# Performance work log

Hardware: AMD Instinct MI355X
Metric: run time of the kernel (lower is better)

## Reference

```python
import jax, jax.numpy as jnp
import numpy as np
import math

_LINK_MASK_VALUE = -1000000000.0
B, N, HID, NH = 8, 1024, 1024, 4
HD = HID // NH


def setup_inputs() -> dict:
    key = jax.random.key(0)
    ks = jax.random.split(key, 8)
    features = jax.random.normal(ks[0], (B, N, HID), dtype=jnp.float32)
    valid_mask = jax.random.bernoulli(ks[1], 0.9, (B, N))
    s = 0.02
    Wq = jax.random.normal(ks[2], (HID, HID), dtype=jnp.float32) * s
    bq = jnp.zeros((HID,), dtype=jnp.float32)
    Wk = jax.random.normal(ks[3], (HID, HID), dtype=jnp.float32) * s
    bk = jnp.zeros((HID,), dtype=jnp.float32)
    Wg = jax.random.normal(ks[4], (HID, NH), dtype=jnp.float32) * s
    bg = jnp.zeros((NH,), dtype=jnp.float32)
    return {"features": features, "valid_mask": valid_mask,
            "Wq": Wq, "bq": bq, "Wk": Wk, "bk": bk, "Wg": Wg, "bg": bg}


def reference(features, valid_mask, Wq, bq, Wk, bk, Wg, bg):
    b, n, _ = features.shape
    Q = (features @ Wq + bq).reshape(b, n, NH, HD)
    K = (features @ Wk + bk).reshape(b, n, NH, HD)
    log_gates = jax.nn.log_softmax(features @ Wg + bg, axis=-1)  # (b, n, H)
    scores = jnp.einsum('bihd,bjhd->bijh', Q, K) / math.sqrt(HD)  # (b, i, j, H)
    triu = jnp.triu(jnp.ones((n, n), dtype=bool), k=1)            # (n, n)
    tvm = triu[None, :, :] & valid_mask[:, None, :]               # (b, i, j)
    row_dead = ~jnp.any(tvm, axis=2, keepdims=True)               # (b, i, 1)
    tvm = tvm | row_dead
    scores = jnp.where(tvm[..., None], scores, _LINK_MASK_VALUE)
    log_per_head = jax.nn.log_softmax(scores, axis=2)             # softmax over j
    log_per_head = jnp.where(row_dead[..., None], _LINK_MASK_VALUE, log_per_head)
    # mixture over heads with per-row gates
    log_links = jax.scipy.special.logsumexp(log_per_head + log_gates[:, :, None, :], axis=-1)
    return log_links
```

## Files before the change

kernel.cpp:

```cpp
#include <hip/hip_runtime.h>


typedef __attribute__((ext_vector_type(8))) short bf16x8;
typedef __attribute__((ext_vector_type(4))) short bf16x4;
typedef __attribute__((ext_vector_type(4))) float f32x4;
typedef __attribute__((ext_vector_type(16))) float f32x16;
typedef __attribute__((ext_vector_type(8))) int i32x8;

#define LB __launch_bounds__(256)

__device__ __forceinline__ short f2bf(float f) {
    unsigned u = __float_as_uint(f);
    u += 0x7fffu + ((u >> 16) & 1u);
    return (short)(u >> 16);
}

__device__ __forceinline__ void gld16(const void* g, void* l) {
    __builtin_amdgcn_global_load_lds(
        (const __attribute__((address_space(1))) unsigned int*)g,
        (__attribute__((address_space(3))) unsigned int*)l, 16, 0, 0);
}

__global__ LB void k_prep2(const float* __restrict__ feat, const float* __restrict__ Wg,
                           const float* __restrict__ bg, const float* __restrict__ Wq,
                           const float* __restrict__ Wk, char* __restrict__ X8,
                           float* __restrict__ lgA, char* __restrict__ W8) {
    __shared__ float tile[32][33];
    const int t = threadIdx.x;
    if (blockIdx.x < 2048) {
        int row = blockIdx.x * 4 + (t >> 6);
        int lane = t & 63;
        const float* f = feat + (size_t)row * 1024;
        float g0 = 0.f, g1 = 0.f, g2 = 0.f, g3 = 0.f;
#pragma unroll
        for (int tt = 0; tt < 4; ++tt) {
            int k = tt * 256 + lane * 4;
            float4 x = *(const float4*)&f[k];
            float4 w0 = *(const float4*)&Wg[(k + 0) * 4];
            float4 w1 = *(const float4*)&Wg[(k + 1) * 4];
            float4 w2 = *(const float4*)&Wg[(k + 2) * 4];
            float4 w3 = *(const float4*)&Wg[(k + 3) * 4];
            g0 += x.x * w0.x + x.y * w1.x + x.z * w2.x + x.w * w3.x;
            g1 += x.x * w0.y + x.y * w1.y + x.z * w2.y + x.w * w3.y;
            g2 += x.x * w0.z + x.y * w1.z + x.z * w2.z + x.w * w3.z;
            g3 += x.x * w0.w + x.y * w1.w + x.z * w2.w + x.w * w3.w;
            unsigned u01 = (unsigned)__builtin_amdgcn_cvt_pk_fp8_f32(x.x, x.y, 0, false);
            unsigned u23 = (unsigned)__builtin_amdgcn_cvt_pk_fp8_f32(x.z, x.w, 0, false);
            *(unsigned*)&X8[(size_t)row * 1024 + k] = (u01 & 0xffffu) | (u23 << 16);
        }
#pragma unroll
        for (int off = 32; off; off >>= 1) {
            g0 += __shfl_xor(g0, off); g1 += __shfl_xor(g1, off);
            g2 += __shfl_xor(g2, off); g3 += __shfl_xor(g3, off);
        }
        g0 += bg[0]; g1 += bg[1]; g2 += bg[2]; g3 += bg[3];
        float m = fmaxf(fmaxf(g0, g1), fmaxf(g2, g3));
        float s = __expf(g0 - m) + __expf(g1 - m) + __expf(g2 - m) + __expf(g3 - m);
        float ls = m + __logf(s);
        if (lane == 0) {
            float4 o = {g0 - ls, g1 - ls, g2 - ls, g3 - ls};
            *(float4*)&lgA[row * 4] = o;
        }
    } else {
        int bid = blockIdx.x - 2048;
        int n0 = (bid & 63) * 32, k0 = (bid >> 6) * 32;
        const float* W = (n0 < 1024) ? Wq : Wk;
        int nb = n0 & 1023;
        int tx = t & 31, ty = t >> 5;
#pragma unroll
        for (int jj = 0; jj < 4; ++jj) {
            int k = ty + jj * 8;
            tile[k][tx] = W[(size_t)(k0 + k) * 1024 + nb + tx];
        }
        __syncthreads();
#pragma unroll
        for (int jj = 0; jj < 4; ++jj) {
            int n = ty + jj * 8;
            float w16 = tile[tx][n] * 16.f;
            W8[(size_t)(n0 + n) * 1024 + k0 + tx] =
                (char)(__builtin_amdgcn_cvt_pk_fp8_f32(w16, w16, 0, false) & 0xff);
        }
    }
}

__device__ __forceinline__ i32x8 ldfrag8(const char* tb, int row, int khalf) {
    const int sw = (row >> 1) & 3;
    uint4 lo = *(const uint4*)&tb[row * 64 + (((khalf * 2 + 0) ^ sw) * 16)];
    uint4 hi = *(const uint4*)&tb[row * 64 + (((khalf * 2 + 1) ^ sw) * 16)];
    i32x8 r;
    r[0] = lo.x; r[1] = lo.y; r[2] = lo.z; r[3] = lo.w;
    r[4] = hi.x; r[5] = hi.y; r[6] = hi.z; r[7] = hi.w;
    return r;
}

__global__ __launch_bounds__(512, 2) void k_gemm(const char* __restrict__ X8,
                                                 const char* __restrict__ W8,
                                                 const float* __restrict__ bq,
                                                 const float* __restrict__ bk,
                                                 short* __restrict__ Qb,
                                                 short* __restrict__ Kb) {
    __shared__ char SM[3][32768];
    const int t = threadIdx.x;
    const int lane = t & 63, wid = t >> 6;
    const int wr = wid >> 2, wc = wid & 3;
    const int l31 = lane & 31, khalf = lane >> 5;
    const int wgid = (blockIdx.x & 7) * 32 + (blockIdx.x >> 3);
    const int m0t = (wgid >> 3) * 256, n0t = (wgid & 7) * 256;

    f32x16 acc[4][2] = {};

#define SGA(q, k1, dst)                                                         \
    { int s_ = (q) * 512 + t; int tr_ = s_ >> 2, c_ = s_ & 3;                   \
      gld16(&X8[(size_t)(m0t + tr_) * 1024 + (k1) + (((c_) ^ ((tr_ >> 1) & 3)) * 16)], \
            (dst) + s_ * 16); }
#define SGB(q, k1, dst)                                                         \
    { int s_ = (q) * 512 + t; int tr_ = s_ >> 2, c_ = s_ & 3;                   \
      gld16(&W8[(size_t)(n0t + tr_) * 1024 + (k1) + (((c_) ^ ((tr_ >> 1) & 3)) * 16)], \
            (dst) + 16384 + s_ * 16); }

    SGA(0, 0, SM[0]); SGA(1, 0, SM[0]); SGB(0, 0, SM[0]); SGB(1, 0, SM[0]);
    SGA(0, 64, SM[1]); SGA(1, 64, SM[1]); SGB(0, 64, SM[1]); SGB(1, 64, SM[1]);
    asm volatile("s_waitcnt vmcnt(4)" ::: "memory");
    __builtin_amdgcn_sched_barrier(0);
    __builtin_amdgcn_s_barrier();

    for (int kt = 0; kt < 16; ++kt) {
        const char* buf = SM[kt % 3];
        char* bufn = SM[(kt + 2) % 3];
        if (kt < 14) {
            const int k2 = (kt + 2) * 64;
            SGA(0, k2, bufn); SGA(1, k2, bufn); SGB(0, k2, bufn); SGB(1, k2, bufn);
        }
        i32x8 aF[4], bF[2];
#pragma unroll
        for (int rt = 0; rt < 4; ++rt)
            aF[rt] = ldfrag8(buf, wr * 128 + rt * 32 + l31, khalf);
#pragma unroll
        for (int ct = 0; ct < 2; ++ct)
            bF[ct] = ldfrag8(buf + 16384, wc * 64 + ct * 32 + l31, khalf);
        __builtin_amdgcn_s_setprio(1);
#pragma unroll
        for (int rt = 0; rt < 4; ++rt)
#pragma unroll
            for (int ct = 0; ct < 2; ++ct)
                acc[rt][ct] = __builtin_amdgcn_mfma_scale_f32_32x32x64_f8f6f4(
                    aF[rt], bF[ct], acc[rt][ct], 0, 0, 0, 127, 0, 127);
        __builtin_amdgcn_s_setprio(0);
        if (kt < 14)       asm volatile("s_waitcnt vmcnt(4)" ::: "memory");
        else if (kt == 14) asm volatile("s_waitcnt vmcnt(0)" ::: "memory");
        __builtin_amdgcn_sched_barrier(0);
        __builtin_amdgcn_s_barrier();
    }
#undef SGA
#undef SGB

#pragma unroll
    for (int rt = 0; rt < 4; ++rt) {
#pragma unroll
        for (int ct = 0; ct < 2; ++ct) {
            const int col = n0t + wc * 64 + ct * 32 + l31;
            const float bias = (col < 1024) ? bq[col] : bk[col - 1024];
            const float scale = (col < 1024) ? 0.0625f : 1.0f;
            short* dst = (col < 1024) ? Qb : Kb;
            const int h = (col >> 8) & 3, d = col & 255;
#pragma unroll
            for (int reg = 0; reg < 16; ++reg) {
                const int rin = (reg & 3) + 8 * (reg >> 2) + 4 * khalf;
                const int grow = m0t + wr * 128 + rt * 32 + rin;
                const int b_ = grow >> 10, i_ = grow & 1023;
                float v = (acc[rt][ct][reg] * 0.0625f + bias) * scale;
                dst[((size_t)(b_ * 4 + h) * 1024 + i_) * 256 + d] = f2bf(v);
            }
        }
    }
}

__global__ __launch_bounds__(256, 2) void k_sc(const short* __restrict__ Qb,
                                               const short* __restrict__ Kb,
                                               const int* __restrict__ vm,
                                               char* __restrict__ Pe8,
                                               float* __restrict__ Zp) {
    __shared__ short SMEM[32768];
    short* As0 = SMEM;
    short* Bs0 = SMEM + 16384;
    const int t = threadIdx.x;
    const int lane = t & 63, wid = t >> 6;
    const int wr = wid >> 1, wc = wid & 1;
    const int lr = lane & 15, lg4 = lane >> 4;
    const int gidx = (blockIdx.x & 7) * 144 + (blockIdx.x >> 3);
    const int bh = gidx / 36, tt = gidx % 36;
    const int it8 = (tt >= 8) + (tt >= 15) + (tt >= 21) + (tt >= 26)
                  + (tt >= 30) + (tt >= 33) + (tt >= 35);
    const int base8 = (it8 == 0) ? 0 : (it8 == 1) ? 8 : (it8 == 2) ? 15
                    : (it8 == 3) ? 21 : (it8 == 4) ? 26 : (it8 == 5) ? 30
                    : (it8 == 6) ? 33 : 35;
    const int jt8 = it8 + (tt - base8);
    const int b = bh >> 2;
    const short* Qp = Qb + ((size_t)bh << 18);
    const short* Kp = Kb + ((size_t)bh << 18);

    f32x4 acc[4][4] = {};

#define SCA(q, k1, dst)                                                         \
    { int s_ = (q) * 256 + t; int tr_ = s_ >> 3, sl_ = s_ & 7;                  \
      gld16(&Qp[(size_t)(it8 * 128 + tr_) * 256 + (k1) + ((sl_ ^ (tr_ & 7)) * 8)], \
            &(dst)[s_ * 8]); }
#define SCB(q, k1, dst)                                                         \
    { int s_ = (q) * 256 + t; int tr_ = s_ >> 3, sl_ = s_ & 7;                  \
      gld16(&Kp[(size_t)(jt8 * 128 + tr_) * 256 + (k1) + ((sl_ ^ (tr_ & 7)) * 8)], \
            &(dst)[s_ * 8]); }

    {
        short* Ad = As0; short* Bd = Bs0;
        SCA(0, 0, Ad); SCA(1, 0, Ad); SCA(2, 0, Ad); SCA(3, 0, Ad);
        SCB(0, 0, Bd); SCB(1, 0, Bd); SCB(2, 0, Bd); SCB(3, 0, Bd);
    }
    asm volatile("s_waitcnt vmcnt(0)" ::: "memory");
    __builtin_amdgcn_sched_barrier(0);
    __builtin_amdgcn_s_barrier();

    for (int kt = 0; kt < 4; ++kt) {
        const int cur = kt & 1;
        const short* Ac = As0 + cur * 8192;
        const short* Bc = Bs0 + cur * 8192;
        short* Ad = As0 + (cur ^ 1) * 8192;
        short* Bd = Bs0 + (cur ^ 1) * 8192;
        const int k1 = (kt + 1) * 64;
        bf16x8 aF[2][2], bF[4][2];
#pragma unroll
        for (int m = 0; m < 2; ++m)
#pragma unroll
            for (int ks = 0; ks < 2; ++ks) {
                int row = wr * 64 + m * 16 + lr;
                aF[m][ks] = *(const bf16x8*)
                    &Ac[row * 64 + (((ks * 4 + lg4) ^ (lr & 7)) * 8)];
            }
#pragma unroll
        for (int n = 0; n < 4; ++n)
#pragma unroll
            for (int ks = 0; ks < 2; ++ks) {
                int row = wc * 64 + n * 16 + lr;
                bF[n][ks] = *(const bf16x8*)
                    &Bc[row * 64 + (((ks * 4 + lg4) ^ (lr & 7)) * 8)];
            }
        if (kt < 3) { SCA(0, k1, Ad); SCA(2, k1, Ad); SCB(0, k1, Bd); SCB(2, k1, Bd); }
        if (kt < 3) asm volatile("s_waitcnt vmcnt(4)" ::: "memory");
        else        asm volatile("s_waitcnt vmcnt(0)" ::: "memory");
        __builtin_amdgcn_sched_barrier(0);
        __builtin_amdgcn_s_barrier();
        asm volatile("s_waitcnt lgkmcnt(0)" ::: "memory");
        __builtin_amdgcn_sched_barrier(0);
        __builtin_amdgcn_s_setprio(1);
#pragma unroll
        for (int ks = 0; ks < 2; ++ks)
#pragma unroll
            for (int m = 0; m < 2; ++m)
#pragma unroll
                for (int n = 0; n < 4; ++n)
                    acc[m][n] = __builtin_amdgcn_mfma_f32_16x16x32_bf16(
                        aF[m][ks], bF[n][ks], acc[m][n], 0, 0, 0);
        __builtin_amdgcn_s_setprio(0);
#pragma unroll
        for (int m = 0; m < 2; ++m)
#pragma unroll
            for (int ks = 0; ks < 2; ++ks) {
                int row = wr * 64 + 32 + m * 16 + lr;
                aF[m][ks] = *(const bf16x8*)
                    &Ac[row * 64 + (((ks * 4 + lg4) ^ (lr & 7)) * 8)];
            }
        if (kt < 3) {
            SCB(1, k1, Bd); SCB(3, k1, Bd); SCA(1, k1, Ad); SCA(3, k1, Ad);
            asm volatile("s_waitcnt vmcnt(2)" ::: "memory");
            __builtin_amdgcn_sched_barrier(0);
        }
        __builtin_amdgcn_s_barrier();
        asm volatile("s_waitcnt lgkmcnt(0)" ::: "memory");
        __builtin_amdgcn_sched_barrier(0);
        __builtin_amdgcn_s_setprio(1);
#pragma unroll
        for (int ks = 0; ks < 2; ++ks)
#pragma unroll
            for (int m = 0; m < 2; ++m)
#pragma unroll
                for (int n = 0; n < 4; ++n)
                    acc[2 + m][n] = __builtin_amdgcn_mfma_f32_16x16x32_bf16(
                        aF[m][ks], bF[n][ks], acc[2 + m][n], 0, 0, 0);
        __builtin_amdgcn_s_setprio(0);
    }
#undef SCA
#undef SCB

    __syncthreads();
    char* wbuf = (char*)SMEM + wid * 5120;
    char* Pp = Pe8 + ((size_t)bh << 20);
    const int rowbase = it8 * 128 + wr * 64;
    const int colbase = jt8 * 128 + wc * 64;
    int vmv[4];
#pragma unroll
    for (int nf = 0; nf < 4; ++nf)
        vmv[nf] = vm[(b << 10) + colbase + nf * 16 + lr];
    float zacc[4][4] = {};
#pragma unroll
    for (int m4 = 0; m4 < 4; ++m4) {
#pragma unroll
        for (int nf = 0; nf < 4; ++nf) {
            const int col = colbase + nf * 16 + lr;
            float e0 = __expf(acc[m4][nf][0]);
            float e1 = __expf(acc[m4][nf][1]);
            float e2 = __expf(acc[m4][nf][2]);
            float e3 = __expf(acc[m4][nf][3]);
            const int row0 = rowbase + m4 * 16 + lg4 * 4;
            zacc[m4][0] += (vmv[nf] && (col > row0 + 0)) ? e0 : 0.f;
            zacc[m4][1] += (vmv[nf] && (col > row0 + 1)) ? e1 : 0.f;
            zacc[m4][2] += (vmv[nf] && (col > row0 + 2)) ? e2 : 0.f;
            zacc[m4][3] += (vmv[nf] && (col > row0 + 3)) ? e3 : 0.f;
            unsigned u01 = (unsigned)__builtin_amdgcn_cvt_pk_fp8_f32(e0, e1, 0, false);
            unsigned u23 = (unsigned)__builtin_amdgcn_cvt_pk_fp8_f32(e2, e3, 0, false);
            const int lrow = m4 * 16 + lg4 * 4;
            const int lcol = nf * 16 + lr;
            wbuf[(lrow + 0) * 80 + lcol] = (char)(u01 & 0xff);
            wbuf[(lrow + 1) * 80 + lcol] = (char)((u01 >> 8) & 0xff);
            wbuf[(lrow + 2) * 80 + lcol] = (char)(u23 & 0xff);
            wbuf[(lrow + 3) * 80 + lcol] = (char)((u23 >> 8) & 0xff);
        }
    }
#pragma unroll
    for (int c = 0; c < 4; ++c) {
        const int rrow = c * 16 + (lane >> 2);
        uint4 v = *(const uint4*)&wbuf[rrow * 80 + (lane & 3) * 16];
        const int grow = rowbase + rrow;
        if (colbase + 63 > grow)
            *(uint4*)&Pp[(size_t)grow * 1024 + colbase + (lane & 3) * 16] = v;
    }
#pragma unroll
    for (int m4 = 0; m4 < 4; ++m4)
#pragma unroll
        for (int r = 0; r < 4; ++r) {
            zacc[m4][r] += __shfl_xor(zacc[m4][r], 1);
            zacc[m4][r] += __shfl_xor(zacc[m4][r], 2);
            zacc[m4][r] += __shfl_xor(zacc[m4][r], 4);
            zacc[m4][r] += __shfl_xor(zacc[m4][r], 8);
        }
    if (lr == 0) {
        float* Zs = Zp + (size_t)(jt8 * 2 + wc) * 32768 + bh * 1024;
#pragma unroll
        for (int m4 = 0; m4 < 4; ++m4)
#pragma unroll
            for (int r = 0; r < 4; ++r)
                Zs[rowbase + m4 * 16 + lg4 * 4 + r] = zacc[m4][r];
    }
}

__global__ LB void k_final(const char* __restrict__ Pe8, const int* __restrict__ vm,
                           const float* __restrict__ lgA, const float* __restrict__ Zp,
                           float* __restrict__ out) {
    __shared__ float ecs[4];
    const int blk = blockIdx.x;
    const int b = blk >> 10, i = blk & 1023;
    const int t = threadIdx.x;
    if (t < 64) {
        int h = t >> 4, sl = t & 15;
        int base = (b * 4 + h) * 1024 + i;
        float z = (sl >= ((i >> 7) << 1)) ? Zp[(size_t)sl * 32768 + base] : 0.f;
        z += __shfl_xor(z, 1); z += __shfl_xor(z, 2);
        z += __shfl_xor(z, 4); z += __shfl_xor(z, 8);
        if (sl == 0) {
            float lgv = lgA[blk * 4 + h];
            ecs[h] = (z > 0.f) ? __expf(lgv) / z : 0.f;
        }
    }
    __syncthreads();
    const int j0 = t * 4;
    float4 o = {-1.0e9f, -1.0e9f, -1.0e9f, -1.0e9f};
    if (j0 + 3 > i) {
        int4 v4 = *(const int4*)&vm[(b << 10) + j0];
        float a0 = 0.f, a1 = 0.f, a2 = 0.f, a3 = 0.f;
#pragma unroll
        for (int h = 0; h < 4; ++h) {
            unsigned p = *(const unsigned*)
                &Pe8[(((size_t)(b * 4 + h)) << 20) + ((size_t)i << 10) + j0];
            float ech = ecs[h];
            a0 += __builtin_amdgcn_cvt_f32_fp8((int)p, 0) * ech;
            a1 += __builtin_amdgcn_cvt_f32_fp8((int)p, 1) * ech;
            a2 += __builtin_amdgcn_cvt_f32_fp8((int)p, 2) * ech;
            a3 += __builtin_amdgcn_cvt_f32_fp8((int)p, 3) * ech;
        }
        o.x = (v4.x && (j0 + 0 > i)) ? __logf(a0) : -1.0e9f;
        o.y = (v4.y && (j0 + 1 > i)) ? __logf(a1) : -1.0e9f;
        o.z = (v4.z && (j0 + 2 > i)) ? __logf(a2) : -1.0e9f;
        o.w = (v4.w && (j0 + 3 > i)) ? __logf(a3) : -1.0e9f;
    }
    *(float4*)&out[((size_t)blk << 10) + j0] = o;
}

extern "C" void kernel_launch(void* const* d_in, const int* in_sizes, int n_in,
                              void* d_out, int out_size, void* d_ws, size_t ws_size,
                              hipStream_t stream) {
    const float* features = (const float*)d_in[0];
    const int*   vmask    = (const int*)d_in[1];
    const float* Wq       = (const float*)d_in[2];
    const float* bq       = (const float*)d_in[3];
    const float* Wk       = (const float*)d_in[4];
    const float* bk       = (const float*)d_in[5];
    const float* Wg       = (const float*)d_in[6];
    const float* bg       = (const float*)d_in[7];
    float* out = (float*)d_out;

    char*  Pe8 = (char*)d_ws;
    char*  X8  = (char*)d_ws;
    char*  W8  = X8 + 8388608;
    short* Qb = (short*)((char*)d_ws + 33554432);
    short* Kb = Qb + 8388608;
    float* lgA = (float*)(Kb + 8388608);
    float* Zp  = lgA + 32768;

    k_prep2<<<4096, 256, 0, stream>>>(features, Wg, bg, Wq, Wk, X8, lgA, W8);
    k_gemm<<<256, 512, 0, stream>>>(X8, W8, bq, bk, Qb, Kb);
    k_sc<<<1152, 256, 0, stream>>>(Qb, Kb, vmask, Pe8, Zp);
    k_final<<<8192, 256, 0, stream>>>(Pe8, vmask, lgA, Zp, out);
}
```

Measured before the change: 80.81 us.

## Store Q/K as FP8 and compute attention scores with FP8 scaled MFMA

```diff
diff --git a/kernel.cpp b/kernel.cpp
--- a/kernel.cpp
+++ b/kernel.cpp
@@ -97,8 +97,8 @@
                                                  const char* __restrict__ W8,
                                                  const float* __restrict__ bq,
                                                  const float* __restrict__ bk,
-                                                 short* __restrict__ Qb,
-                                                 short* __restrict__ Kb) {
+                                                 char* __restrict__ Q8,
+                                                 char* __restrict__ K8) {
     __shared__ char SM[3][32768];
     const int t = threadIdx.x;
     const int lane = t & 63, wid = t >> 6;
@@ -160,33 +160,43 @@
         for (int ct = 0; ct < 2; ++ct) {
             const int col = n0t + wc * 64 + ct * 32 + l31;
             const float bias = (col < 1024) ? bq[col] : bk[col - 1024];
-            const float scale = (col < 1024) ? 0.0625f : 1.0f;
-            short* dst = (col < 1024) ? Qb : Kb;
+            char* dst = (col < 1024) ? Q8 : K8;
             const int h = (col >> 8) & 3, d = col & 255;
 #pragma unroll
             for (int reg = 0; reg < 16; ++reg) {
                 const int rin = (reg & 3) + 8 * (reg >> 2) + 4 * khalf;
                 const int grow = m0t + wr * 128 + rt * 32 + rin;
                 const int b_ = grow >> 10, i_ = grow & 1023;
-                float v = (acc[rt][ct][reg] * 0.0625f + bias) * scale;
-                dst[((size_t)(b_ * 4 + h) * 1024 + i_) * 256 + d] = f2bf(v);
+                float v = acc[rt][ct][reg] * 0.0625f + bias;
+                dst[((size_t)(b_ * 4 + h) * 1024 + i_) * 256 + d] =
+                    (char)(__builtin_amdgcn_cvt_pk_fp8_f32(v, v, 0, false) & 0xff);
             }
         }
     }
 }
 
-__global__ __launch_bounds__(256, 2) void k_sc(const short* __restrict__ Qb,
-                                               const short* __restrict__ Kb,
+__device__ __forceinline__ i32x8 ldsc(const char* tb, int row, int p0) {
+    const int sw = row & 15;
+    uint4 lo = *(const uint4*)&tb[row * 256 + (((p0 + 0) ^ sw) * 16)];
+    uint4 hi = *(const uint4*)&tb[row * 256 + (((p0 + 1) ^ sw) * 16)];
+    i32x8 r;
+    r[0] = lo.x; r[1] = lo.y; r[2] = lo.z; r[3] = lo.w;
+    r[4] = hi.x; r[5] = hi.y; r[6] = hi.z; r[7] = hi.w;
+    return r;
+}
+
+__global__ __launch_bounds__(256, 2) void k_sc(const char* __restrict__ Q8,
+                                               const char* __restrict__ K8,
                                                const int* __restrict__ vm,
                                                char* __restrict__ Pe8,
                                                float* __restrict__ Zp) {
-    __shared__ short SMEM[32768];
-    short* As0 = SMEM;
-    short* Bs0 = SMEM + 16384;
+    __shared__ char SMEM[65536];
+    char* As = SMEM;
+    char* Bs = SMEM + 32768;
     const int t = threadIdx.x;
     const int lane = t & 63, wid = t >> 6;
     const int wr = wid >> 1, wc = wid & 1;
-    const int lr = lane & 15, lg4 = lane >> 4;
+    const int l31 = lane & 31, khalf = lane >> 5;
     const int gidx = (blockIdx.x & 7) * 144 + (blockIdx.x >> 3);
     const int bh = gidx / 36, tt = gidx % 36;
     const int it8 = (tt >= 8) + (tt >= 15) + (tt >= 21) + (tt >= 26)
@@ -196,132 +206,72 @@
                     : (it8 == 6) ? 33 : 35;
     const int jt8 = it8 + (tt - base8);
     const int b = bh >> 2;
-    const short* Qp = Qb + ((size_t)bh << 18);
-    const short* Kp = Kb + ((size_t)bh << 18);
-
-    f32x4 acc[4][4] = {};
-
-#define SCA(q, k1, dst)                                                         \
-    { int s_ = (q) * 256 + t; int tr_ = s_ >> 3, sl_ = s_ & 7;                  \
-      gld16(&Qp[(size_t)(it8 * 128 + tr_) * 256 + (k1) + ((sl_ ^ (tr_ & 7)) * 8)], \
-            &(dst)[s_ * 8]); }
-#define SCB(q, k1, dst)                                                         \
-    { int s_ = (q) * 256 + t; int tr_ = s_ >> 3, sl_ = s_ & 7;                  \
-      gld16(&Kp[(size_t)(jt8 * 128 + tr_) * 256 + (k1) + ((sl_ ^ (tr_ & 7)) * 8)], \
-            &(dst)[s_ * 8]); }
-
-    {
-        short* Ad = As0; short* Bd = Bs0;
-        SCA(0, 0, Ad); SCA(1, 0, Ad); SCA(2, 0, Ad); SCA(3, 0, Ad);
-        SCB(0, 0, Bd); SCB(1, 0, Bd); SCB(2, 0, Bd); SCB(3, 0, Bd);
+    const char* Qp = Q8 + ((size_t)bh << 18);
+    const char* Kp = K8 + ((size_t)bh << 18);
+
+#pragma unroll
+    for (int pass = 0; pass < 8; ++pass) {
+        int s_ = pass * 256 + t;
+        int row = s_ >> 4, g = s_ & 15;
+        gld16(&Qp[(size_t)(it8 * 128 + row) * 256 + ((g ^ (row & 15)) * 16)],
+              As + s_ * 16);
+    }
+#pragma unroll
+    for (int pass = 0; pass < 8; ++pass) {
+        int s_ = pass * 256 + t;
+        int row = s_ >> 4, g = s_ & 15;
+        gld16(&Kp[(size_t)(jt8 * 128 + row) * 256 + ((g ^ (row & 15)) * 16)],
+              Bs + s_ * 16);
     }
     asm volatile("s_waitcnt vmcnt(0)" ::: "memory");
     __builtin_amdgcn_sched_barrier(0);
     __builtin_amdgcn_s_barrier();
 
-    for (int kt = 0; kt < 4; ++kt) {
-        const int cur = kt & 1;
-        const short* Ac = As0 + cur * 8192;
-        const short* Bc = Bs0 + cur * 8192;
-        short* Ad = As0 + (cur ^ 1) * 8192;
-        short* Bd = Bs0 + (cur ^ 1) * 8192;
-        const int k1 = (kt + 1) * 64;
-        bf16x8 aF[2][2], bF[4][2];
-#pragma unroll
-        for (int m = 0; m < 2; ++m)
-#pragma unroll
-            for (int ks = 0; ks < 2; ++ks) {
-                int row = wr * 64 + m * 16 + lr;
-                aF[m][ks] = *(const bf16x8*)
-                    &Ac[row * 64 + (((ks * 4 + lg4) ^ (lr & 7)) * 8)];
-            }
-#pragma unroll
-        for (int n = 0; n < 4; ++n)
-#pragma unroll
-            for (int ks = 0; ks < 2; ++ks) {
-                int row = wc * 64 + n * 16 + lr;
-                bF[n][ks] = *(const bf16x8*)
-                    &Bc[row * 64 + (((ks * 4 + lg4) ^ (lr & 7)) * 8)];
-            }
-        if (kt < 3) { SCA(0, k1, Ad); SCA(2, k1, Ad); SCB(0, k1, Bd); SCB(2, k1, Bd); }
-        if (kt < 3) asm volatile("s_waitcnt vmcnt(4)" ::: "memory");
-        else        asm volatile("s_waitcnt vmcnt(0)" ::: "memory");
-        __builtin_amdgcn_sched_barrier(0);
-        __builtin_amdgcn_s_barrier();
-        asm volatile("s_waitcnt lgkmcnt(0)" ::: "memory");
-        __builtin_amdgcn_sched_barrier(0);
+    f32x16 acc[2][2] = {};
+#pragma unroll
+    for (int ks = 0; ks < 4; ++ks) {
+        const int p0 = ks * 4 + khalf * 2;
+        i32x8 aF[2], bF[2];
+#pragma unroll
+        for (int rt = 0; rt < 2; ++rt)
+            aF[rt] = ldsc(As, wr * 64 + rt * 32 + l31, p0);
+#pragma unroll
+        for (int ct = 0; ct < 2; ++ct)
+            bF[ct] = ldsc(Bs, wc * 64 + ct * 32 + l31, p0);
         __builtin_amdgcn_s_setprio(1);
 #pragma unroll
-        for (int ks = 0; ks < 2; ++ks)
-#pragma unroll
-            for (int m = 0; m < 2; ++m)
-#pragma unroll
-                for (int n = 0; n < 4; ++n)
-                    acc[m][n] = __builtin_amdgcn_mfma_f32_16x16x32_bf16(
-                        aF[m][ks], bF[n][ks], acc[m][n], 0, 0, 0);
+        for (int rt = 0; rt < 2; ++rt)
+#pragma unroll
+            for (int ct = 0; ct < 2; ++ct)
+                acc[rt][ct] = __builtin_amdgcn_mfma_scale_f32_32x32x64_f8f6f4(
+                    aF[rt], bF[ct], acc[rt][ct], 0, 0, 0, 127, 0, 127);
         __builtin_amdgcn_s_setprio(0);
-#pragma unroll
-        for (int m = 0; m < 2; ++m)
-#pragma unroll
-            for (int ks = 0; ks < 2; ++ks) {
-                int row = wr * 64 + 32 + m * 16 + lr;
-                aF[m][ks] = *(const bf16x8*)
-                    &Ac[row * 64 + (((ks * 4 + lg4) ^ (lr & 7)) * 8)];
-            }
-        if (kt < 3) {
-            SCB(1, k1, Bd); SCB(3, k1, Bd); SCA(1, k1, Ad); SCA(3, k1, Ad);
-            asm volatile("s_waitcnt vmcnt(2)" ::: "memory");
-            __builtin_amdgcn_sched_barrier(0);
-        }
-        __builtin_amdgcn_s_barrier();
-        asm volatile("s_waitcnt lgkmcnt(0)" ::: "memory");
-        __builtin_amdgcn_sched_barrier(0);
-        __builtin_amdgcn_s_setprio(1);
-#pragma unroll
-        for (int ks = 0; ks < 2; ++ks)
-#pragma unroll
-            for (int m = 0; m < 2; ++m)
-#pragma unroll
-                for (int n = 0; n < 4; ++n)
-                    acc[2 + m][n] = __builtin_amdgcn_mfma_f32_16x16x32_bf16(
-                        aF[m][ks], bF[n][ks], acc[2 + m][n], 0, 0, 0);
-        __builtin_amdgcn_s_setprio(0);
-    }
-#undef SCA
-#undef SCB
+    }
 
     __syncthreads();
-    char* wbuf = (char*)SMEM + wid * 5120;
+    char* wbuf = SMEM + wid * 5120;
     char* Pp = Pe8 + ((size_t)bh << 20);
     const int rowbase = it8 * 128 + wr * 64;
     const int colbase = jt8 * 128 + wc * 64;
-    int vmv[4];
-#pragma unroll
-    for (int nf = 0; nf < 4; ++nf)
-        vmv[nf] = vm[(b << 10) + colbase + nf * 16 + lr];
-    float zacc[4][4] = {};
-#pragma unroll
-    for (int m4 = 0; m4 < 4; ++m4) {
-#pragma unroll
-        for (int nf = 0; nf < 4; ++nf) {
-            const int col = colbase + nf * 16 + lr;
-            float e0 = __expf(acc[m4][nf][0]);
-            float e1 = __expf(acc[m4][nf][1]);
-            float e2 = __expf(acc[m4][nf][2]);
-            float e3 = __expf(acc[m4][nf][3]);
-            const int row0 = rowbase + m4 * 16 + lg4 * 4;
-            zacc[m4][0] += (vmv[nf] && (col > row0 + 0)) ? e0 : 0.f;
-            zacc[m4][1] += (vmv[nf] && (col > row0 + 1)) ? e1 : 0.f;
-            zacc[m4][2] += (vmv[nf] && (col > row0 + 2)) ? e2 : 0.f;
-            zacc[m4][3] += (vmv[nf] && (col > row0 + 3)) ? e3 : 0.f;
-            unsigned u01 = (unsigned)__builtin_amdgcn_cvt_pk_fp8_f32(e0, e1, 0, false);
-            unsigned u23 = (unsigned)__builtin_amdgcn_cvt_pk_fp8_f32(e2, e3, 0, false);
-            const int lrow = m4 * 16 + lg4 * 4;
-            const int lcol = nf * 16 + lr;
-            wbuf[(lrow + 0) * 80 + lcol] = (char)(u01 & 0xff);
-            wbuf[(lrow + 1) * 80 + lcol] = (char)((u01 >> 8) & 0xff);
-            wbuf[(lrow + 2) * 80 + lcol] = (char)(u23 & 0xff);
-            wbuf[(lrow + 3) * 80 + lcol] = (char)((u23 >> 8) & 0xff);
+    int vmv[2];
+#pragma unroll
+    for (int ct = 0; ct < 2; ++ct)
+        vmv[ct] = vm[(b << 10) + colbase + ct * 32 + l31];
+    float zacc[2][16] = {};
+#pragma unroll
+    for (int rt = 0; rt < 2; ++rt) {
+#pragma unroll
+        for (int ct = 0; ct < 2; ++ct) {
+            const int col = colbase + ct * 32 + l31;
+#pragma unroll
+            for (int reg = 0; reg < 16; ++reg) {
+                const int rin = (reg & 3) + 8 * (reg >> 2) + 4 * khalf;
+                const int row = rowbase + rt * 32 + rin;
+                float e = __expf(acc[rt][ct][reg] * 0.0625f);
+                zacc[rt][reg] += (vmv[ct] && (col > row)) ? e : 0.f;
+                wbuf[(rt * 32 + rin) * 80 + ct * 32 + l31] =
+                    (char)(__builtin_amdgcn_cvt_pk_fp8_f32(e, e, 0, false) & 0xff);
+            }
         }
     }
 #pragma unroll
@@ -333,21 +283,24 @@
             *(uint4*)&Pp[(size_t)grow * 1024 + colbase + (lane & 3) * 16] = v;
     }
 #pragma unroll
-    for (int m4 = 0; m4 < 4; ++m4)
-#pragma unroll
-        for (int r = 0; r < 4; ++r) {
-            zacc[m4][r] += __shfl_xor(zacc[m4][r], 1);
-            zacc[m4][r] += __shfl_xor(zacc[m4][r], 2);
-            zacc[m4][r] += __shfl_xor(zacc[m4][r], 4);
-            zacc[m4][r] += __shfl_xor(zacc[m4][r], 8);
-        }
-    if (lr == 0) {
+    for (int rt = 0; rt < 2; ++rt)
+#pragma unroll
+        for (int reg = 0; reg < 16; ++reg) {
+            zacc[rt][reg] += __shfl_xor(zacc[rt][reg], 1);
+            zacc[rt][reg] += __shfl_xor(zacc[rt][reg], 2);
+            zacc[rt][reg] += __shfl_xor(zacc[rt][reg], 4);
+            zacc[rt][reg] += __shfl_xor(zacc[rt][reg], 8);
+            zacc[rt][reg] += __shfl_xor(zacc[rt][reg], 16);
+        }
+    if (l31 == 0) {
         float* Zs = Zp + (size_t)(jt8 * 2 + wc) * 32768 + bh * 1024;
 #pragma unroll
-        for (int m4 = 0; m4 < 4; ++m4)
-#pragma unroll
-            for (int r = 0; r < 4; ++r)
-                Zs[rowbase + m4 * 16 + lg4 * 4 + r] = zacc[m4][r];
+        for (int rt = 0; rt < 2; ++rt)
+#pragma unroll
+            for (int reg = 0; reg < 16; ++reg) {
+                const int rin = (reg & 3) + 8 * (reg >> 2) + 4 * khalf;
+                Zs[rowbase + rt * 32 + rin] = zacc[rt][reg];
+            }
     }
 }
 
@@ -409,13 +362,13 @@
     char*  Pe8 = (char*)d_ws;
     char*  X8  = (char*)d_ws;
     char*  W8  = X8 + 8388608;
-    short* Qb = (short*)((char*)d_ws + 33554432);
-    short* Kb = Qb + 8388608;
-    float* lgA = (float*)(Kb + 8388608);
+    char*  Q8  = (char*)d_ws + 33554432;
+    char*  K8  = Q8 + 8388608;
+    float* lgA = (float*)(K8 + 8388608);
     float* Zp  = lgA + 32768;
 
     k_prep2<<<4096, 256, 0, stream>>>(features, Wg, bg, Wq, Wk, X8, lgA, W8);
-    k_gemm<<<256, 512, 0, stream>>>(X8, W8, bq, bk, Qb, Kb);
-    k_sc<<<1152, 256, 0, stream>>>(Qb, Kb, vmask, Pe8, Zp);
+    k_gemm<<<256, 512, 0, stream>>>(X8, W8, bq, bk, Q8, K8);
+    k_sc<<<1152, 256, 0, stream>>>(Q8, K8, vmask, Pe8, Zp);
     k_final<<<8192, 256, 0, stream>>>(Pe8, vmask, lgA, Zp, out);
 }
```

Result: faster. 76.58 us (median of 3 runs) (-5.2%).
